# Optimization experiments

Measured on AMD Instinct MI355X. Metric: run time of the kernel, lower is better.

Reference implementation:

```python
import jax, jax.numpy as jnp
import numpy as np

BIG_NEG = -1000000000.0
B, N, X, D = 16, 32, 36, 2048
H = 512

def setup_inputs() -> dict:
    key = jax.random.key(0)
    ks = jax.random.split(key, 16)
    inp = {
        'fc_feats_target': jax.random.normal(ks[0], (B, 1, D), jnp.float32),
        'fc_feats_distr': jax.random.normal(ks[1], (B, N, D), jnp.float32),
        'att_feats_target': jax.random.normal(ks[2], (B, 1, X, D), jnp.float32),
        'att_feats_distr': jax.random.normal(ks[3], (B, N, X, D), jnp.float32),
        'att_masks_target': jax.random.randint(ks[4], (B, 1, X), 0, 2, jnp.int32),
        'att_masks_distr': jax.random.randint(ks[5], (B, N, X), 0, 2, jnp.int32),
        # scorer MLP params: Linear(2D->H), Linear(H->1)
        'W1': jax.random.normal(ks[6], (2 * D, H), jnp.float32) * 0.02,
        'b1': jnp.zeros((H,), jnp.float32),
        'W2': jax.random.normal(ks[7], (H, 1), jnp.float32) * 0.02,
        'b2': jnp.zeros((1,), jnp.float32),
        # bilinear weight, initialized to identity as in the module
        'Wbil': jnp.eye(D, dtype=jnp.float32),
        # object_scorer MLP params
        'oW1': jax.random.normal(ks[8], (2 * D, H), jnp.float32) * 0.02,
        'ob1': jnp.zeros((H,), jnp.float32),
        'oW2': jax.random.normal(ks[9], (H, 1), jnp.float32) * 0.02,
        'ob2': jnp.zeros((1,), jnp.float32),
    }
    return inp

def _mlp(x, W1, b1, W2, b2):
    h = jax.nn.relu(x @ W1 + b1)
    return (h @ W2 + b2)[..., 0]  # squeeze(-1)

def reference(fc_feats_target, fc_feats_distr, att_feats_target, att_feats_distr,
              att_masks_target, att_masks_distr,
              W1, b1, W2, b2, Wbil, oW1, ob1, oW2, ob2):
    # base scorer on global (fc) features
    ft = jnp.broadcast_to(fc_feats_target, fc_feats_distr.shape)  # [B,N,D]
    cat_feats = jnp.concatenate([ft, fc_feats_distr], axis=-1)    # [B,N,2D]
    scores = _mlp(cat_feats, W1, b1, W2, b2)                      # [B,N]

    # bilinear compatibility: einsum('bixd,biye,de->bixy') with target broadcast over i
    tproj = jnp.einsum('bxd,de->bxe', att_feats_target[:, 0], Wbil)        # [B,X,D]
    inners = jnp.einsum('bxd,biyd->bixy', tproj, att_feats_distr)          # [B,N,X,Y]

    mask_outer = (att_masks_target[:, 0][:, None, :, None]
                  * att_masks_distr[:, :, None, :])                        # [B,N,X,Y]
    inners = jnp.where(mask_outer > 0, inners, BIG_NEG)

    target_weights = jax.nn.softmax(jnp.max(inners, axis=3), axis=-1)      # [B,N,X]
    distr_weights = jax.nn.softmax(jnp.max(inners, axis=2), axis=-1)       # [B,N,Y]

    target_feats = jnp.einsum('bxd,bix->bid', att_feats_target[:, 0], target_weights)
    distr_feats = jnp.einsum('biyd,biy->bid', att_feats_distr, distr_weights)

    cat_att = jnp.concatenate([target_feats, distr_feats], axis=-1)        # [B,N,2D]
    scores = scores + _mlp(cat_att, oW1, ob1, oW2, ob2)

    return jax.nn.log_softmax(scores, axis=-1)  # [B,N]
```

## Files before the change

### kernel.cpp

```cpp
#include <hip/hip_runtime.h>
#include <math.h>

#define D_   2048
#define H_   512
#define K2D  4096
#define X_   36
#define NCOL 1152

#define Z_MLP 32
#define Z_TP  8
#define Z_S   4

#define O_A   0u
#define O_B   9437184u
#define O_SB  11534336u
#define O_SO  11534848u

#define SP_PLANE 663552u

typedef __attribute__((ext_vector_type(8))) short bf8_t;
typedef __attribute__((ext_vector_type(4))) float f4_t;

__device__ __forceinline__ unsigned short f2bf(float f) {
  unsigned u = __float_as_uint(f);
  unsigned r = u + 0x7FFFu + ((u >> 16) & 1u);
  return (unsigned short)(r >> 16);
}
__device__ __forceinline__ float bf2f(unsigned short h) {
  return __uint_as_float(((unsigned)h) << 16);
}

#define TSTR 40

__device__ __forceinline__ void cvt8(unsigned short* Hp, unsigned short* Lp,
                                     float4 a, float4 b) {
  __align__(16) unsigned short h[8], l[8];
  float x[8] = {a.x, a.y, a.z, a.w, b.x, b.y, b.z, b.w};
  #pragma unroll
  for (int j = 0; j < 8; j++) {
    h[j] = f2bf(x[j]);
    l[j] = f2bf(x[j] - bf2f(h[j]));
  }
  *(bf8_t*)Hp = *(bf8_t*)&h[0];
  *(bf8_t*)Lp = *(bf8_t*)&l[0];
}

__global__ __launch_bounds__(256, 4) void gemm_mfma64(
    const float* __restrict__ A, const float* __restrict__ A2,
    const float* __restrict__ Bm, float* __restrict__ Cpart,
    int M, int N, int K, int kchunk, int amode)
{
  __shared__ __align__(16) unsigned short AsH[64 * TSTR], AsL[64 * TSTR];
  __shared__ __align__(16) unsigned short BsH[64 * TSTR], BsL[64 * TSTR];
  const int t  = threadIdx.x;
  const int m0 = blockIdx.y << 6;
  const int n0 = blockIdx.x << 6;
  const int k0 = blockIdx.z * kchunk;
  const int kend = k0 + kchunk;
  const int w  = t >> 6;
  const int ln = t & 15;
  const int qd = (t >> 4) & 3;
  const int wm = (w >> 1) << 5;
  const int wn = (w & 1) << 5;
  const int a_row = t >> 2;
  const int a_kq  = (t & 3) << 3;
  const int b_col = t & 63;
  const int b_kq  = (t >> 6) << 3;

  f4_t acc[2][2];
  #pragma unroll
  for (int i = 0; i < 2; i++)
    #pragma unroll
    for (int j = 0; j < 2; j++) acc[i][j] = (f4_t)0.f;

  float4 pa0, pa1;
  float  pb[8];

  auto loadA = [&](int kb) {
    int gr = m0 + a_row;
    int gk = kb + a_kq;
    pa0 = make_float4(0.f, 0.f, 0.f, 0.f);
    pa1 = pa0;
    if (gr < M) {
      const float* src;
      if (amode == 0) src = A + (size_t)gr * K + gk;
      else src = (gk < 2048) ? (A  + ((size_t)(gr >> 5) << 11) + gk)
                             : (A2 + ((size_t)gr << 11) + (gk - 2048));
      pa0 = *(const float4*)src;
      pa1 = *(const float4*)(src + 4);
    }
  };
  auto loadB = [&](int kb) {
    #pragma unroll
    for (int j = 0; j < 8; j++)
      pb[j] = Bm[(size_t)(kb + b_kq + j) * N + n0 + b_col];
  };

  loadA(k0); loadB(k0);

  for (int kb = k0; kb < kend; kb += 32) {
    __syncthreads();
    cvt8(&AsH[a_row * TSTR + a_kq], &AsL[a_row * TSTR + a_kq], pa0, pa1);
    cvt8(&BsH[b_col * TSTR + b_kq], &BsL[b_col * TSTR + b_kq],
         make_float4(pb[0], pb[1], pb[2], pb[3]),
         make_float4(pb[4], pb[5], pb[6], pb[7]));
    __syncthreads();
    if (kb + 32 < kend) { loadA(kb + 32); loadB(kb + 32); }
    bf8_t ah[2], al[2], bh[2], bl[2];
    #pragma unroll
    for (int fm = 0; fm < 2; fm++) {
      int r = (wm + (fm << 4) + ln) * TSTR + (qd << 3);
      ah[fm] = *(const bf8_t*)&AsH[r];
      al[fm] = *(const bf8_t*)&AsL[r];
    }
    #pragma unroll
    for (int fn = 0; fn < 2; fn++) {
      int r = (wn + (fn << 4) + ln) * TSTR + (qd << 3);
      bh[fn] = *(const bf8_t*)&BsH[r];
      bl[fn] = *(const bf8_t*)&BsL[r];
    }
    #pragma unroll
    for (int fm = 0; fm < 2; fm++)
      #pragma unroll
      for (int fn = 0; fn < 2; fn++) {
        acc[fm][fn] = __builtin_amdgcn_mfma_f32_16x16x32_bf16(ah[fm], bh[fn], acc[fm][fn], 0, 0, 0);
        acc[fm][fn] = __builtin_amdgcn_mfma_f32_16x16x32_bf16(ah[fm], bl[fn], acc[fm][fn], 0, 0, 0);
        acc[fm][fn] = __builtin_amdgcn_mfma_f32_16x16x32_bf16(al[fm], bh[fn], acc[fm][fn], 0, 0, 0);
      }
  }
  float* Cz = Cpart + (size_t)blockIdx.z * M * N;
  #pragma unroll
  for (int fm = 0; fm < 2; fm++) {
    #pragma unroll
    for (int reg = 0; reg < 4; reg++) {
      int gr = m0 + wm + (fm << 4) + (qd << 2) + reg;
      if (gr < M) {
        #pragma unroll
        for (int fn = 0; fn < 2; fn++)
          Cz[(size_t)gr * N + n0 + wn + (fn << 4) + ln] = acc[fm][fn][reg];
      }
    }
  }
}

__global__ __launch_bounds__(256) void reduce_tp(
    const float* __restrict__ tpp, float* __restrict__ tproj)
{
  int idx = blockIdx.x * 256 + threadIdx.x;
  const float4* p = (const float4*)tpp;
  float4 a = p[idx];
  #pragma unroll
  for (int z = 1; z < Z_TP; z++) {
    float4 b = p[idx + (size_t)z * 294912];
    a.x += b.x; a.y += b.y; a.z += b.z; a.w += b.w;
  }
  ((float4*)tproj)[idx] = a;
}

__global__ __launch_bounds__(256, 4) void sgemm36_mfma(
    const float* __restrict__ tproj, const float* __restrict__ attd,
    float* __restrict__ Spart, int kchunk)
{
  __shared__ __align__(16) unsigned short AsH[48 * TSTR], AsL[48 * TSTR];
  __shared__ __align__(16) unsigned short BsH[64 * TSTR], BsL[64 * TSTR];
  const int t  = threadIdx.x;
  const int n0 = blockIdx.x << 6;
  const int b  = blockIdx.y;
  const int k0 = blockIdx.z * kchunk;
  const int kend = k0 + kchunk;
  const int w  = t >> 6;
  const int ln = t & 15;
  const int qd = (t >> 4) & 3;
  const float* Ab = tproj + (size_t)b * X_ * D_;
  const float* Bb = attd  + (size_t)b * NCOL * D_;
  const int a_row = t >> 2;
  const int a_kq  = (t & 3) << 3;
  const int b_col = t & 63;
  const int b_kq  = (t >> 6) << 3;

  f4_t acc[3];
  #pragma unroll
  for (int i = 0; i < 3; i++) acc[i] = (f4_t)0.f;

  float4 pa0, pa1, pb0, pb1;

  auto loadA = [&](int kb) {
    pa0 = make_float4(0.f, 0.f, 0.f, 0.f);
    pa1 = pa0;
    if (a_row < X_) {
      const float* src = Ab + (size_t)a_row * D_ + kb + a_kq;
      pa0 = *(const float4*)src;
      pa1 = *(const float4*)(src + 4);
    }
  };
  auto loadB = [&](int kb) {
    const float* src = Bb + (size_t)(n0 + b_col) * D_ + kb + b_kq;
    pb0 = *(const float4*)src;
    pb1 = *(const float4*)(src + 4);
  };

  loadA(k0); loadB(k0);

  for (int kb = k0; kb < kend; kb += 32) {
    __syncthreads();
    if (a_row < 48)
      cvt8(&AsH[a_row * TSTR + a_kq], &AsL[a_row * TSTR + a_kq], pa0, pa1);
    cvt8(&BsH[b_col * TSTR + b_kq], &BsL[b_col * TSTR + b_kq], pb0, pb1);
    __syncthreads();
    if (kb + 32 < kend) { loadA(kb + 32); loadB(kb + 32); }
    bf8_t ah[3], al[3], bh, bl;
    #pragma unroll
    for (int fm = 0; fm < 3; fm++) {
      int r = ((fm << 4) + ln) * TSTR + (qd << 3);
      ah[fm] = *(const bf8_t*)&AsH[r];
      al[fm] = *(const bf8_t*)&AsL[r];
    }
    {
      int r = ((w << 4) + ln) * TSTR + (qd << 3);
      bh = *(const bf8_t*)&BsH[r];
      bl = *(const bf8_t*)&BsL[r];
    }
    #pragma unroll
    for (int fm = 0; fm < 3; fm++) {
      acc[fm] = __builtin_amdgcn_mfma_f32_16x16x32_bf16(ah[fm], bh, acc[fm], 0, 0, 0);
      acc[fm] = __builtin_amdgcn_mfma_f32_16x16x32_bf16(ah[fm], bl, acc[fm], 0, 0, 0);
      acc[fm] = __builtin_amdgcn_mfma_f32_16x16x32_bf16(al[fm], bh, acc[fm], 0, 0, 0);
    }
  }
  float* Sz = Spart + (size_t)blockIdx.z * SP_PLANE + (size_t)b * X_ * NCOL;
  #pragma unroll
  for (int fm = 0; fm < 3; fm++) {
    #pragma unroll
    for (int reg = 0; reg < 4; reg++) {
      int x = (fm << 4) + (qd << 2) + reg;
      if (x < X_)
        Sz[(size_t)x * NCOL + n0 + (w << 4) + ln] = acc[fm][reg];
    }
  }
}

__global__ __launch_bounds__(256) void mlp_tail_z(
    const float* __restrict__ hp, const float* __restrict__ b1,
    const float* __restrict__ w2, const float* __restrict__ b2,
    float* __restrict__ out)
{
  int row = blockIdx.x;
  int t   = threadIdx.x;
  float v = 0.f;
  #pragma unroll
  for (int q = 0; q < 2; q++) {
    int h = t + (q << 8);
    float s = 0.f;
    #pragma unroll
    for (int z = 0; z < Z_MLP; z++)
      s += hp[(size_t)z * (H_ * 512) + (size_t)row * H_ + h];
    s += b1[h];
    v += fmaxf(s, 0.f) * w2[h];
  }
  #pragma unroll
  for (int off = 32; off > 0; off >>= 1) v += __shfl_down(v, off, 64);
  __shared__ float red[4];
  if ((t & 63) == 0) red[t >> 6] = v;
  __syncthreads();
  if (t == 0) out[row] = red[0] + red[1] + red[2] + red[3] + b2[0];
}

__global__ __launch_bounds__(256) void attn_fused(
    const float* __restrict__ Spart, const int* __restrict__ amt,
    const int* __restrict__ amd, const float* __restrict__ attt,
    const float* __restrict__ attd, float* __restrict__ cat)
{
  __shared__ float Sm[36 * 37];
  __shared__ int   mtv[36], mdv[36];
  __shared__ float mrow[36], mcol[36], twl[36], dwl[36];
  int bi = blockIdx.x;
  int b  = bi >> 5;
  int i  = bi & 31;
  int t  = threadIdx.x;
  if (t < 36) { mtv[t] = amt[b * 36 + t]; mdv[t] = amd[bi * 36 + t]; }
  __syncthreads();
  for (int f = t; f < 324; f += 256) {
    int x  = f / 9;
    int yq = (f - x * 9) << 2;
    size_t o = (((size_t)b * X_ + x) * NCOL + i * 36 + yq) >> 2;
    const float4* p = (const float4*)Spart;
    float4 v = p[o];
    #pragma unroll
    for (int z = 1; z < Z_S; z++) {
      float4 wv = p[o + ((size_t)z * SP_PLANE >> 2)];
      v.x += wv.x; v.y += wv.y; v.z += wv.z; v.w += wv.w;
    }
    float* dst = &Sm[x * 37 + yq];
    bool mx = (mtv[x] != 0);
    dst[0] = (mx && mdv[yq + 0] != 0) ? v.x : -1e9f;
    dst[1] = (mx && mdv[yq + 1] != 0) ? v.y : -1e9f;
    dst[2] = (mx && mdv[yq + 2] != 0) ? v.z : -1e9f;
    dst[3] = (mx && mdv[yq + 3] != 0) ? v.w : -1e9f;
  }
  __syncthreads();
  if (t < 36) {
    float r = -INFINITY, c = -INFINITY;
    for (int k = 0; k < 36; k++) {
      r = fmaxf(r, Sm[t * 37 + k]);
      c = fmaxf(c, Sm[k * 37 + t]);
    }
    mrow[t] = r; mcol[t] = c;
  }
  __syncthreads();
  if (t < 64) {
    float v = (t < 36) ? mrow[t] : -INFINITY;
    float m = v;
    #pragma unroll
    for (int off = 32; off > 0; off >>= 1) m = fmaxf(m, __shfl_xor(m, off, 64));
    float e = (t < 36) ? expf(v - m) : 0.f;
    float s = e;
    #pragma unroll
    for (int off = 32; off > 0; off >>= 1) s += __shfl_xor(s, off, 64);
    if (t < 36) twl[t] = e / s;
  } else if (t < 128) {
    int l = t - 64;
    float v = (l < 36) ? mcol[l] : -INFINITY;
    float m = v;
    #pragma unroll
    for (int off = 32; off > 0; off >>= 1) m = fmaxf(m, __shfl_xor(m, off, 64));
    float e = (l < 36) ? expf(v - m) : 0.f;
    float s = e;
    #pragma unroll
    for (int off = 32; off > 0; off >>= 1) s += __shfl_xor(s, off, 64);
    if (l < 36) dwl[l] = e / s;
  }
  __syncthreads();
  const float4* at4 = (const float4*)(attt + (size_t)b * X_ * D_);
  const float4* ad4 = (const float4*)(attd + (size_t)bi * X_ * D_);
  float4 t0 = make_float4(0, 0, 0, 0), t1 = t0, d0 = t0, d1 = t0;
  for (int x = 0; x < 36; x++) {
    float wt = twl[x], wd = dwl[x];
    float4 a  = at4[x * 512 + t];
    float4 a2 = at4[x * 512 + t + 256];
    float4 e  = ad4[x * 512 + t];
    float4 e2 = ad4[x * 512 + t + 256];
    t0.x = fmaf(wt, a.x, t0.x);  t0.y = fmaf(wt, a.y, t0.y);
    t0.z = fmaf(wt, a.z, t0.z);  t0.w = fmaf(wt, a.w, t0.w);
    t1.x = fmaf(wt, a2.x, t1.x); t1.y = fmaf(wt, a2.y, t1.y);
    t1.z = fmaf(wt, a2.z, t1.z); t1.w = fmaf(wt, a2.w, t1.w);
    d0.x = fmaf(wd, e.x, d0.x);  d0.y = fmaf(wd, e.y, d0.y);
    d0.z = fmaf(wd, e.z, d0.z);  d0.w = fmaf(wd, e.w, d0.w);
    d1.x = fmaf(wd, e2.x, d1.x); d1.y = fmaf(wd, e2.y, d1.y);
    d1.z = fmaf(wd, e2.z, d1.z); d1.w = fmaf(wd, e2.w, d1.w);
  }
  float4* c4 = (float4*)(cat + (size_t)bi * K2D);
  c4[t] = t0; c4[t + 256] = t1; c4[512 + t] = d0; c4[512 + t + 256] = d1;
}

__global__ __launch_bounds__(64) void lsm(
    const float* __restrict__ sb, const float* __restrict__ so,
    float* __restrict__ out)
{
  int b = blockIdx.x, t = threadIdx.x;
  float s = (t < 32) ? sb[b * 32 + t] + so[b * 32 + t] : -INFINITY;
  float m = s;
  #pragma unroll
  for (int off = 32; off > 0; off >>= 1) m = fmaxf(m, __shfl_xor(m, off, 64));
  float e = (t < 32) ? expf(s - m) : 0.f;
  float sum = e;
  #pragma unroll
  for (int off = 32; off > 0; off >>= 1) sum += __shfl_xor(sum, off, 64);
  if (t < 32) out[b * 32 + t] = s - m - logf(sum);
}

extern "C" void kernel_launch(void* const* d_in, const int* in_sizes, int n_in,
                              void* d_out, int out_size, void* d_ws, size_t ws_size,
                              hipStream_t stream)
{
  const float* fc_t  = (const float*)d_in[0];
  const float* fc_d  = (const float*)d_in[1];
  const float* att_t = (const float*)d_in[2];
  const float* att_d = (const float*)d_in[3];
  const int*   am_t  = (const int*)d_in[4];
  const int*   am_d  = (const int*)d_in[5];
  const float* W1    = (const float*)d_in[6];
  const float* b1    = (const float*)d_in[7];
  const float* W2    = (const float*)d_in[8];
  const float* b2    = (const float*)d_in[9];
  const float* Wbil  = (const float*)d_in[10];
  const float* oW1   = (const float*)d_in[11];
  const float* ob1   = (const float*)d_in[12];
  const float* oW2   = (const float*)d_in[13];
  const float* ob2   = (const float*)d_in[14];
  float* ws  = (float*)d_ws;
  float* out = (float*)d_out;

  gemm_mfma64<<<dim3(8, 8, Z_MLP), 256, 0, stream>>>(fc_t, fc_d, W1, ws + O_A,
                                                     512, 512, 4096, 4096 / Z_MLP, 1);
  mlp_tail_z<<<512, 256, 0, stream>>>(ws + O_A, b1, W2, b2, ws + O_SB);
  gemm_mfma64<<<dim3(32, 9, Z_TP), 256, 0, stream>>>(att_t, nullptr, Wbil, ws + O_A,
                                                     576, 2048, 2048, 2048 / Z_TP, 0);
  reduce_tp<<<1152, 256, 0, stream>>>(ws + O_A, ws + O_B);
  sgemm36_mfma<<<dim3(18, 16, Z_S), 256, 0, stream>>>(ws + O_B, att_d, ws + O_A,
                                                      2048 / Z_S);
  attn_fused<<<512, 256, 0, stream>>>(ws + O_A, am_t, am_d, att_t, att_d, ws + O_B);
  gemm_mfma64<<<dim3(8, 8, Z_MLP), 256, 0, stream>>>(ws + O_B, nullptr, oW1, ws + O_A,
                                                     512, 512, 4096, 4096 / Z_MLP, 0);
  mlp_tail_z<<<512, 256, 0, stream>>>(ws + O_A, ob1, oW2, ob2, ws + O_SO);
  lsm<<<16, 64, 0, stream>>>(ws + O_SB, ws + O_SO, out);
}
```

Measured before the change: 392.8 us.

## Fuse bilinear score GEMM into attention kernel with pre-split bf16 target projection

Removes the separate split-K score GEMM and its partial-sum buffer, and computes each (b,i) 36x36 score tile directly inside the attention kernel. The four waves each take a K-quarter and reduce through shared memory. reduce_tp now emits the target projection already split into bf16 hi/lo planes, so the per-block conversion of A is avoided. This cuts one launch and the global round trip of the score partials. In exchange each block does a longer serial K loop with register-only prefetch and no shared-memory tiling, and the target rows are reloaded by all 32 distractor blocks of the same batch.

```diff
diff --git a/kernel.cpp b/kernel.cpp
--- a/kernel.cpp
+++ b/kernel.cpp
@@ -9,14 +9,12 @@
 
 #define Z_MLP 32
 #define Z_TP  8
-#define Z_S   4
 
 #define O_A   0u
 #define O_B   9437184u
 #define O_SB  11534336u
 #define O_SO  11534848u
-
-#define SP_PLANE 663552u
+#define O_C   11536384u
 
 typedef __attribute__((ext_vector_type(8))) short bf8_t;
 typedef __attribute__((ext_vector_type(4))) float f4_t;
@@ -43,6 +41,18 @@
   }
   *(bf8_t*)Hp = *(bf8_t*)&h[0];
   *(bf8_t*)Lp = *(bf8_t*)&l[0];
+}
+
+__device__ __forceinline__ void cvt8v(bf8_t* H, bf8_t* L, float4 a, float4 b) {
+  float x[8] = {a.x, a.y, a.z, a.w, b.x, b.y, b.z, b.w};
+  bf8_t hh, ll;
+  #pragma unroll
+  for (int j = 0; j < 8; j++) {
+    unsigned short h = f2bf(x[j]);
+    hh[j] = (short)h;
+    ll[j] = (short)f2bf(x[j] - bf2f(h));
+  }
+  *H = hh; *L = ll;
 }
 
 __global__ __launch_bounds__(256, 4) void gemm_mfma64(
@@ -144,7 +154,8 @@
 }
 
 __global__ __launch_bounds__(256) void reduce_tp(
-    const float* __restrict__ tpp, float* __restrict__ tproj)
+    const float* __restrict__ tpp, unsigned short* __restrict__ tH,
+    unsigned short* __restrict__ tL)
 {
   int idx = blockIdx.x * 256 + threadIdx.x;
   const float4* p = (const float4*)tpp;
@@ -154,89 +165,13 @@
     float4 b = p[idx + (size_t)z * 294912];
     a.x += b.x; a.y += b.y; a.z += b.z; a.w += b.w;
   }
-  ((float4*)tproj)[idx] = a;
-}
-
-__global__ __launch_bounds__(256, 4) void sgemm36_mfma(
-    const float* __restrict__ tproj, const float* __restrict__ attd,
-    float* __restrict__ Spart, int kchunk)
-{
-  __shared__ __align__(16) unsigned short AsH[48 * TSTR], AsL[48 * TSTR];
-  __shared__ __align__(16) unsigned short BsH[64 * TSTR], BsL[64 * TSTR];
-  const int t  = threadIdx.x;
-  const int n0 = blockIdx.x << 6;
-  const int b  = blockIdx.y;
-  const int k0 = blockIdx.z * kchunk;
-  const int kend = k0 + kchunk;
-  const int w  = t >> 6;
-  const int ln = t & 15;
-  const int qd = (t >> 4) & 3;
-  const float* Ab = tproj + (size_t)b * X_ * D_;
-  const float* Bb = attd  + (size_t)b * NCOL * D_;
-  const int a_row = t >> 2;
-  const int a_kq  = (t & 3) << 3;
-  const int b_col = t & 63;
-  const int b_kq  = (t >> 6) << 3;
-
-  f4_t acc[3];
-  #pragma unroll
-  for (int i = 0; i < 3; i++) acc[i] = (f4_t)0.f;
-
-  float4 pa0, pa1, pb0, pb1;
-
-  auto loadA = [&](int kb) {
-    pa0 = make_float4(0.f, 0.f, 0.f, 0.f);
-    pa1 = pa0;
-    if (a_row < X_) {
-      const float* src = Ab + (size_t)a_row * D_ + kb + a_kq;
-      pa0 = *(const float4*)src;
-      pa1 = *(const float4*)(src + 4);
-    }
-  };
-  auto loadB = [&](int kb) {
-    const float* src = Bb + (size_t)(n0 + b_col) * D_ + kb + b_kq;
-    pb0 = *(const float4*)src;
-    pb1 = *(const float4*)(src + 4);
-  };
-
-  loadA(k0); loadB(k0);
-
-  for (int kb = k0; kb < kend; kb += 32) {
-    __syncthreads();
-    if (a_row < 48)
-      cvt8(&AsH[a_row * TSTR + a_kq], &AsL[a_row * TSTR + a_kq], pa0, pa1);
-    cvt8(&BsH[b_col * TSTR + b_kq], &BsL[b_col * TSTR + b_kq], pb0, pb1);
-    __syncthreads();
-    if (kb + 32 < kend) { loadA(kb + 32); loadB(kb + 32); }
-    bf8_t ah[3], al[3], bh, bl;
-    #pragma unroll
-    for (int fm = 0; fm < 3; fm++) {
-      int r = ((fm << 4) + ln) * TSTR + (qd << 3);
-      ah[fm] = *(const bf8_t*)&AsH[r];
-      al[fm] = *(const bf8_t*)&AsL[r];
-    }
-    {
-      int r = ((w << 4) + ln) * TSTR + (qd << 3);
-      bh = *(const bf8_t*)&BsH[r];
-      bl = *(const bf8_t*)&BsL[r];
-    }
-    #pragma unroll
-    for (int fm = 0; fm < 3; fm++) {
-      acc[fm] = __builtin_amdgcn_mfma_f32_16x16x32_bf16(ah[fm], bh, acc[fm], 0, 0, 0);
-      acc[fm] = __builtin_amdgcn_mfma_f32_16x16x32_bf16(ah[fm], bl, acc[fm], 0, 0, 0);
-      acc[fm] = __builtin_amdgcn_mfma_f32_16x16x32_bf16(al[fm], bh, acc[fm], 0, 0, 0);
-    }
-  }
-  float* Sz = Spart + (size_t)blockIdx.z * SP_PLANE + (size_t)b * X_ * NCOL;
-  #pragma unroll
-  for (int fm = 0; fm < 3; fm++) {
-    #pragma unroll
-    for (int reg = 0; reg < 4; reg++) {
-      int x = (fm << 4) + (qd << 2) + reg;
-      if (x < X_)
-        Sz[(size_t)x * NCOL + n0 + (w << 4) + ln] = acc[fm][reg];
-    }
-  }
+  ushort4 h, l;
+  h.x = f2bf(a.x); l.x = f2bf(a.x - bf2f(h.x));
+  h.y = f2bf(a.y); l.y = f2bf(a.y - bf2f(h.y));
+  h.z = f2bf(a.z); l.z = f2bf(a.z - bf2f(h.z));
+  h.w = f2bf(a.w); l.w = f2bf(a.w - bf2f(h.w));
+  ((ushort4*)tH)[idx] = h;
+  ((ushort4*)tL)[idx] = l;
 }
 
 __global__ __launch_bounds__(256) void mlp_tail_z(
@@ -265,44 +200,102 @@
   if (t == 0) out[row] = red[0] + red[1] + red[2] + red[3] + b2[0];
 }
 
-__global__ __launch_bounds__(256) void attn_fused(
-    const float* __restrict__ Spart, const int* __restrict__ amt,
-    const int* __restrict__ amd, const float* __restrict__ attt,
-    const float* __restrict__ attd, float* __restrict__ cat)
-{
-  __shared__ float Sm[36 * 37];
+__global__ __launch_bounds__(256, 2) void attn_bi(
+    const unsigned short* __restrict__ tH,
+    const float* __restrict__ attd,
+    const int* __restrict__ amt, const int* __restrict__ amd,
+    const float* __restrict__ attt, float* __restrict__ cat)
+{
+  __shared__ float Sp[4][36][37];
   __shared__ int   mtv[36], mdv[36];
   __shared__ float mrow[36], mcol[36], twl[36], dwl[36];
-  int bi = blockIdx.x;
-  int b  = bi >> 5;
-  int i  = bi & 31;
-  int t  = threadIdx.x;
+  const int bi = blockIdx.x;
+  const int b  = bi >> 5;
+  const int t  = threadIdx.x;
+  const int w  = t >> 6;
+  const int ln = t & 15;
+  const int qd = (t >> 4) & 3;
   if (t < 36) { mtv[t] = amt[b * 36 + t]; mdv[t] = amd[bi * 36 + t]; }
-  __syncthreads();
-  for (int f = t; f < 324; f += 256) {
-    int x  = f / 9;
-    int yq = (f - x * 9) << 2;
-    size_t o = (((size_t)b * X_ + x) * NCOL + i * 36 + yq) >> 2;
-    const float4* p = (const float4*)Spart;
-    float4 v = p[o];
-    #pragma unroll
-    for (int z = 1; z < Z_S; z++) {
-      float4 wv = p[o + ((size_t)z * SP_PLANE >> 2)];
-      v.x += wv.x; v.y += wv.y; v.z += wv.z; v.w += wv.w;
-    }
-    float* dst = &Sm[x * 37 + yq];
-    bool mx = (mtv[x] != 0);
-    dst[0] = (mx && mdv[yq + 0] != 0) ? v.x : -1e9f;
-    dst[1] = (mx && mdv[yq + 1] != 0) ? v.y : -1e9f;
-    dst[2] = (mx && mdv[yq + 2] != 0) ? v.z : -1e9f;
-    dst[3] = (mx && mdv[yq + 3] != 0) ? v.w : -1e9f;
+
+  const unsigned short* tLo = tH + 1179648;
+  const int kw = (w << 9) + (qd << 3);
+  const unsigned short* AH[3];
+  const unsigned short* AL[3];
+  const float* BP[3];
+  #pragma unroll
+  for (int f = 0; f < 3; f++) {
+    int r = f * 16 + ln; if (r > 35) r = 35;
+    size_t ao = ((size_t)b * X_ + r) * D_ + kw;
+    AH[f] = tH  + ao;
+    AL[f] = tLo + ao;
+    BP[f] = attd + ((size_t)bi * X_ + r) * D_ + kw;
+  }
+
+  f4_t acc[3][3];
+  #pragma unroll
+  for (int i = 0; i < 3; i++)
+    #pragma unroll
+    for (int j = 0; j < 3; j++) acc[i][j] = (f4_t)0.f;
+
+  bf8_t ah[3], al[3];
+  float4 pb0[3], pb1[3];
+  #pragma unroll
+  for (int f = 0; f < 3; f++) {
+    ah[f]  = *(const bf8_t*)AH[f];
+    al[f]  = *(const bf8_t*)AL[f];
+    pb0[f] = *(const float4*)BP[f];
+    pb1[f] = *(const float4*)(BP[f] + 4);
+  }
+
+  for (int kk = 0; kk < 16; kk++) {
+    bf8_t bh[3], bl[3], cah[3], cal[3];
+    #pragma unroll
+    for (int f = 0; f < 3; f++) {
+      cvt8v(&bh[f], &bl[f], pb0[f], pb1[f]);
+      cah[f] = ah[f]; cal[f] = al[f];
+    }
+    if (kk < 15) {
+      const int off = (kk + 1) << 5;
+      #pragma unroll
+      for (int f = 0; f < 3; f++) {
+        ah[f]  = *(const bf8_t*)(AH[f] + off);
+        al[f]  = *(const bf8_t*)(AL[f] + off);
+        pb0[f] = *(const float4*)(BP[f] + off);
+        pb1[f] = *(const float4*)(BP[f] + off + 4);
+      }
+    }
+    #pragma unroll
+    for (int fm = 0; fm < 3; fm++)
+      #pragma unroll
+      for (int fn = 0; fn < 3; fn++) {
+        acc[fm][fn] = __builtin_amdgcn_mfma_f32_16x16x32_bf16(cah[fm], bh[fn], acc[fm][fn], 0, 0, 0);
+        acc[fm][fn] = __builtin_amdgcn_mfma_f32_16x16x32_bf16(cah[fm], bl[fn], acc[fm][fn], 0, 0, 0);
+        acc[fm][fn] = __builtin_amdgcn_mfma_f32_16x16x32_bf16(cal[fm], bh[fn], acc[fm][fn], 0, 0, 0);
+      }
+  }
+
+  #pragma unroll
+  for (int fm = 0; fm < 3; fm++)
+    #pragma unroll
+    for (int fn = 0; fn < 3; fn++)
+      #pragma unroll
+      for (int reg = 0; reg < 4; reg++) {
+        int x = (fm << 4) + (qd << 2) + reg;
+        int y = (fn << 4) + ln;
+        if (x < 36 && y < 36) Sp[w][x][y] = acc[fm][fn][reg];
+      }
+  __syncthreads();
+  for (int e = t; e < 1296; e += 256) {
+    int x = e / 36, y = e - x * 36;
+    float v = Sp[0][x][y] + Sp[1][x][y] + Sp[2][x][y] + Sp[3][x][y];
+    Sp[0][x][y] = (mtv[x] != 0 && mdv[y] != 0) ? v : -1e9f;
   }
   __syncthreads();
   if (t < 36) {
     float r = -INFINITY, c = -INFINITY;
     for (int k = 0; k < 36; k++) {
-      r = fmaxf(r, Sm[t * 37 + k]);
-      c = fmaxf(c, Sm[k * 37 + t]);
+      r = fmaxf(r, Sp[0][t][k]);
+      c = fmaxf(c, Sp[0][k][t]);
     }
     mrow[t] = r; mcol[t] = c;
   }
@@ -395,11 +388,11 @@
   mlp_tail_z<<<512, 256, 0, stream>>>(ws + O_A, b1, W2, b2, ws + O_SB);
   gemm_mfma64<<<dim3(32, 9, Z_TP), 256, 0, stream>>>(att_t, nullptr, Wbil, ws + O_A,
                                                      576, 2048, 2048, 2048 / Z_TP, 0);
-  reduce_tp<<<1152, 256, 0, stream>>>(ws + O_A, ws + O_B);
-  sgemm36_mfma<<<dim3(18, 16, Z_S), 256, 0, stream>>>(ws + O_B, att_d, ws + O_A,
-                                                      2048 / Z_S);
-  attn_fused<<<512, 256, 0, stream>>>(ws + O_A, am_t, am_d, att_t, att_d, ws + O_B);
-  gemm_mfma64<<<dim3(8, 8, Z_MLP), 256, 0, stream>>>(ws + O_B, nullptr, oW1, ws + O_A,
+  reduce_tp<<<1152, 256, 0, stream>>>(ws + O_A, (unsigned short*)(ws + O_B),
+                                      (unsigned short*)(ws + O_B) + 1179648);
+  attn_bi<<<512, 256, 0, stream>>>((const unsigned short*)(ws + O_B), att_d,
+                                   am_t, am_d, att_t, ws + O_C);
+  gemm_mfma64<<<dim3(8, 8, Z_MLP), 256, 0, stream>>>(ws + O_C, nullptr, oW1, ws + O_A,
                                                      512, 512, 4096, 4096 / Z_MLP, 0);
   mlp_tail_z<<<512, 256, 0, stream>>>(ws + O_A, ob1, oW2, ob2, ws + O_SO);
   lsm<<<16, 64, 0, stream>>>(ws + O_SB, ws + O_SO, out);
```

After: 375.8 us. 1.05x faster.
